# Kernel tuning notes

Hardware: AMD Instinct MI355X
Metric: run time of the kernel (lower is better)

The kernel has to match this reference:

```python
import math
import jax, jax.numpy as jnp
import numpy as np

# Dims (match init_kwargs)
B, S, HID = 2, 2048, 2048
H, KVH, D = 16, 8, 128
ATTN_H = 8                      # softmax heads (head_split_dict)
TN_H = H - ATTN_H               # linear (tnorm) heads
N_REP = H // KVH                # GQA repeat factor
FIRST_TOKENS, LAST_TOKENS = 64, 512  # global prefix + band width for custom mask
EPS = 1e-6
ROPE_BASE = 1e6
SCALE = 1.0 / math.sqrt(D)


def _rope_tables(seq_len):
    inv_freq = 1.0 / (ROPE_BASE ** (jnp.arange(0, D, 2, dtype=jnp.float32) / D))
    t = jnp.arange(seq_len, dtype=jnp.float32)
    freqs = jnp.outer(t, inv_freq)                 # [S, D/2]
    emb = jnp.concatenate([freqs, freqs], axis=-1)  # [S, D]
    return jnp.cos(emb), jnp.sin(emb)


def _rotate_half(x):
    x1, x2 = jnp.split(x, 2, axis=-1)
    return jnp.concatenate([-x2, x1], axis=-1)


def _apply_rope(x, cos, sin):
    # x: [B, h, S, D], cos/sin: [S, D]
    return x * cos[None, None] + _rotate_half(x) * sin[None, None]


def _rms_norm(x):
    # SimpleRMSNorm: computed in fp32, no learned weight
    xf = x.astype(jnp.float32)
    out = xf * jax.lax.rsqrt(jnp.mean(xf * xf, axis=-1, keepdims=True) + EPS)
    return out.astype(x.dtype)


def setup_inputs() -> dict:
    key = jax.random.key(0)
    ks = jax.random.split(key, 6)
    sc = 0.02
    perm_np = np.array([3, 7, 0, 12, 9, 15, 1, 5, 2, 4, 6, 8, 10, 11, 13, 14], np.int32)
    inv_np = np.zeros(H, np.int32)
    inv_np[perm_np] = np.arange(H, dtype=np.int32)
    return {
        'hidden_states': jax.random.normal(ks[0], (B, S, HID), jnp.float32),
        'q_w': jax.random.normal(ks[1], (HID, HID), jnp.float32) * sc,
        'q_b': jnp.zeros((HID,), jnp.float32),
        'k_w': jax.random.normal(ks[2], (KVH * D, HID), jnp.float32) * sc,
        'k_b': jnp.zeros((KVH * D,), jnp.float32),
        'v_w': jax.random.normal(ks[3], (KVH * D, HID), jnp.float32) * sc,
        'v_b': jnp.zeros((KVH * D,), jnp.float32),
        'o_w': jax.random.normal(ks[4], (HID, HID), jnp.float32) * sc,
        'head_policy': jnp.array([1, 0, 1, 0, 1, 0, 1, 0], dtype=bool),
        'perm': jnp.asarray(perm_np),
        'inv_perm': jnp.asarray(inv_np),
    }


def _custom_mask(head_policy):
    # create_custom_causal_mask: banded causal + global prefix for heads with
    # policy==False; plain causal for heads with policy==True. Additive mask.
    qi = jnp.arange(S)[:, None]
    ki = jnp.arange(S)[None, :]
    causal = ki <= qi
    band = causal & ((qi - ki) < LAST_TOKENS)
    band = band | ((ki < FIRST_TOKENS) & (qi >= FIRST_TOKENS))
    neg = jnp.finfo(jnp.float32).min
    orig = jnp.where(causal, 0.0, neg)
    new = jnp.where(band, 0.0, neg)
    return jnp.where(head_policy[:, None, None], orig, new), causal  # [ATTN_H,S,S]


def reference(hidden_states, q_w, q_b, k_w, k_b, v_w, v_b, o_w,
              head_policy, perm, inv_perm):
    dt = hidden_states.dtype
    q = hidden_states @ q_w.T + q_b           # [B,S,HID]
    k = hidden_states @ k_w.T + k_b           # [B,S,KVH*D]
    v = hidden_states @ v_w.T + v_b

    # head permutation on q, then split softmax vs tnorm heads
    q = q.reshape(B, S, H, D)[:, :, perm, :]
    q = jnp.transpose(q, (0, 2, 1, 3))        # [B,H,S,D]
    kh = jnp.transpose(k.reshape(B, S, KVH, D), (0, 2, 1, 3))  # [B,KVH,S,D]
    vh = jnp.transpose(v.reshape(B, S, KVH, D), (0, 2, 1, 3))

    cos, sin = _rope_tables(S)
    q = _apply_rope(q, cos, sin)              # rope on all q heads (both branches)
    kh = _apply_rope(kh, cos, sin)

    # repeat_kv (GQA) then head permutation
    k_all = jnp.repeat(kh, N_REP, axis=1)[:, perm]  # [B,H,S,D]
    v_all = jnp.repeat(vh, N_REP, axis=1)[:, perm]

    # ---- softmax branch (first ATTN_H heads), custom banded/global mask ----
    mask, causal = _custom_mask(head_policy)
    logits = jnp.einsum('bhqd,bhkd->bhqk', q[:, :ATTN_H], k_all[:, :ATTN_H]) * SCALE
    logits = logits + mask[None]
    probs = jax.nn.softmax(logits.astype(jnp.float32), axis=-1).astype(dt)
    out_sm = jnp.einsum('bhqk,bhkd->bhqd', probs, v_all[:, :ATTN_H])
    out_sm = jnp.transpose(out_sm, (0, 2, 1, 3)).reshape(B, S, ATTN_H * D)

    # ---- linear (tnorm) branch (remaining heads): masked qk^T @ v + RMSNorm ----
    w = jnp.einsum('bhqd,bhkd->bhqk', q[:, ATTN_H:], k_all[:, ATTN_H:]) * SCALE
    w = jnp.where(causal[None, None], w, jnp.zeros((), dt))
    out_tn = jnp.einsum('bhqk,bhkd->bhqd', w, v_all[:, ATTN_H:])
    out_tn = jnp.transpose(out_tn, (0, 2, 1, 3)).reshape(B, S, TN_H * D)
    out_tn = _rms_norm(out_tn)

    # concat heads, undo permutation, output projection
    out = jnp.concatenate([out_sm, out_tn], axis=-1)
    out = out.reshape(B, S, H, D)[:, :, inv_perm, :].reshape(B, S, HID)
    return out @ o_w.T
```

## Files before the change

### kernel.cpp

```cpp
#include <hip/hip_runtime.h>
#include <hip/hip_bf16.h>
#include <stdint.h>

#define AS1 __attribute__((address_space(1)))
#define AS3 __attribute__((address_space(3)))

typedef __bf16 bf16x8 __attribute__((ext_vector_type(8)));
typedef unsigned short u16x8 __attribute__((ext_vector_type(8)));
typedef float f32x4 __attribute__((ext_vector_type(4)));

static __device__ __forceinline__ unsigned short f2bf(float f) {
  unsigned u = __float_as_uint(f);
  u += 0x7fffu + ((u >> 16) & 1u);
  return (unsigned short)(u >> 16);
}
static __device__ __forceinline__ float bf2f(unsigned short h) {
  return __uint_as_float(((unsigned)h) << 16);
}
static __device__ __forceinline__ bf16x8 ld_frag(const unsigned short* p) {
  union { u16x8 u; bf16x8 b; } c;
  c.u = *(const u16x8*)p;
  return c.b;
}
static __device__ __forceinline__ void gload16(const void* g, void* l) {
  __builtin_amdgcn_global_load_lds((AS1 const void*)g, (AS3 void*)l, 16, 0, 0);
}
#define MFMA(a, b, c) __builtin_amdgcn_mfma_f32_16x16x32_bf16(a, b, c, 0, 0, 0)
#define BAR asm volatile("s_barrier" ::: "memory")
#define VM4 asm volatile("s_waitcnt vmcnt(4)" ::: "memory")

__global__ __launch_bounds__(256)
void cvt4(const float* __restrict__ in, unsigned short* __restrict__ out, long n) {
  long i = ((long)blockIdx.x * 256 + threadIdx.x) * 4;
  if (i >= n) return;
  float4 f = *(const float4*)&in[i];
  ushort4 u;
  u.x = f2bf(f.x); u.y = f2bf(f.y); u.z = f2bf(f.z); u.w = f2bf(f.w);
  *(ushort4*)&out[i] = u;
}

__global__ __launch_bounds__(256)
void rope_apply(unsigned short* __restrict__ qh, unsigned short* __restrict__ kh) {
  long i = (long)blockIdx.x * 256 + threadIdx.x;
  const long QT = (long)2 * 16 * 2048 * 64;
  unsigned short* p; long rem; float outsc;
  if (i < QT) { p = qh; rem = i; outsc = 0.08838834764831845f; }
  else        { p = kh; rem = i - QT; outsc = 1.0f; }
  int j = (int)(rem & 63);
  long row = rem >> 6;
  int s = (int)(row & 2047);
  unsigned short* x = p + row * 128;
  float inv = exp2f(-0.31143075889569023f * (float)j);
  float f = (float)s * inv;
  float sn, c;
  sincosf(f, &sn, &c);
  float x1 = bf2f(x[j]), x2 = bf2f(x[j + 64]);
  x[j]      = f2bf((x1 * c - x2 * sn) * outsc);
  x[j + 64] = f2bf((x2 * c + x1 * sn) * outsc);
}

__global__ __launch_bounds__(512, 2)
void gemm256_qkv(const unsigned short* __restrict__ A,
                 const unsigned short* __restrict__ Bw,
                 const float* __restrict__ qb, const float* __restrict__ kb,
                 const float* __restrict__ vb,
                 unsigned short* __restrict__ qh, unsigned short* __restrict__ kh,
                 unsigned short* __restrict__ vT) {
  constexpr int K = 2048, NT = K / 64, NIT = NT / 2;
  __shared__ alignas(16) unsigned short LDS[65536];
  const int id = blockIdx.x;
  const int lg = (id & 7) * 32 + (id >> 3);
  const int bm = lg >> 4, bn = lg & 15;
  const int tid = threadIdx.x;
  const int wid = tid >> 6, lane = tid & 63;
  const int wr = wid >> 2, wc = wid & 3;
  const int l15 = lane & 15, lhi = lane >> 4;
  const int rsw = (l15 & 7) << 3;
  const int srow0 = wid * 8 + (lane >> 3);
  const int scol = ((lane & 7) ^ (lane >> 3)) * 8;
  const unsigned short* Ag = A + (long)(bm * 256) * K;
  const unsigned short* Bg = Bw + (long)(bn * 256) * K;
  unsigned short* Al = LDS;
  unsigned short* Bl = LDS + 32768;

#define STG(gb, lb, p, h, t) do {                                              \
    int tc = (t) < NT ? (t) : NT - 1;                                          \
    gload16((gb) + (long)((h) * 128 + srow0) * K + tc * 64 + scol,             \
            (lb) + (p) * 16384 + (h) * 8192 + wid * 512);                      \
    gload16((gb) + (long)((h) * 128 + 64 + srow0) * K + tc * 64 + scol,        \
            (lb) + (p) * 16384 + (h) * 8192 + 4096 + wid * 512);               \
  } while (0)

#define LDA(p, mh) do {                                                        \
    _Pragma("unroll") for (int m4 = 0; m4 < 4; ++m4)                           \
    _Pragma("unroll") for (int kk = 0; kk < 2; ++kk)                           \
      afr[m4][kk] = ld_frag(&Al[(p) * 16384 +                                  \
          (wr * 128 + (mh) * 64 + m4 * 16 + l15) * 64 +                        \
          ((kk * 32 + lhi * 8) ^ rsw)]);                                       \
  } while (0)

#define LDB(p, nh) do {                                                        \
    _Pragma("unroll") for (int n2 = 0; n2 < 2; ++n2)                           \
    _Pragma("unroll") for (int kk = 0; kk < 2; ++kk)                           \
      bfr[nh][n2][kk] = ld_frag(&Bl[(p) * 16384 +                              \
          (wc * 64 + (nh) * 32 + n2 * 16 + l15) * 64 +                         \
          ((kk * 32 + lhi * 8) ^ rsw)]);                                       \
  } while (0)

#define QUAD(mh, nh) do {                                                      \
    __builtin_amdgcn_s_setprio(1);                                             \
    _Pragma("unroll") for (int m4 = 0; m4 < 4; ++m4)                           \
    _Pragma("unroll") for (int n2 = 0; n2 < 2; ++n2)                           \
    _Pragma("unroll") for (int kk = 0; kk < 2; ++kk)                           \
      acc[(mh) * 4 + m4][(nh) * 2 + n2] =                                      \
          MFMA(afr[m4][kk], bfr[nh][n2][kk], acc[(mh) * 4 + m4][(nh) * 2 + n2]);\
    __builtin_amdgcn_s_setprio(0);                                             \
  } while (0)

  f32x4 acc[8][4] = {};
  bf16x8 afr[4][2], bfr[2][2][2];

  STG(Bg, Bl, 0, 0, 0); STG(Bg, Bl, 0, 1, 0);
  STG(Ag, Al, 0, 0, 0); STG(Ag, Al, 0, 1, 0);
  STG(Bg, Bl, 1, 0, 1); STG(Bg, Bl, 1, 1, 1);
  VM4; BAR;

  for (int it = 0; it < NIT; ++it) {
    const int T = 2 * it;
    LDA(0, 0); LDB(0, 0); STG(Ag, Al, 1, 0, T + 1);
    BAR; QUAD(0, 0); BAR;
    LDB(0, 1);            STG(Ag, Al, 1, 1, T + 1);
    BAR; QUAD(0, 1); BAR;
    LDA(0, 1);            STG(Bg, Bl, 0, 0, T + 2);
    BAR; QUAD(1, 0); BAR;
                          STG(Bg, Bl, 0, 1, T + 2);
    VM4; BAR; QUAD(1, 1); BAR;
    LDA(1, 0); LDB(1, 0); STG(Ag, Al, 0, 0, T + 2);
    BAR; QUAD(0, 0); BAR;
    LDB(1, 1);            STG(Ag, Al, 0, 1, T + 2);
    BAR; QUAD(0, 1); BAR;
    LDA(1, 1);            STG(Bg, Bl, 1, 0, T + 3);
    BAR; QUAD(1, 0); BAR;
                          STG(Bg, Bl, 1, 1, T + 3);
    VM4; BAR; QUAD(1, 1); BAR;
  }

  const int r0 = bm * 256 + wr * 128, c0 = bn * 256 + wc * 64;
#pragma unroll
  for (int m = 0; m < 8; ++m) {
#pragma unroll
    for (int n = 0; n < 4; ++n) {
#pragma unroll
      for (int j = 0; j < 4; ++j) {
        int row = r0 + m * 16 + lhi * 4 + j;
        int col = c0 + n * 16 + l15;
        float v = acc[m][n][j];
        int b = row >> 11, s = row & 2047;
        if (col < 2048) {
          v += qb[col];
          qh[((long)(b * 16 + (col >> 7)) * 2048 + s) * 128 + (col & 127)] = f2bf(v);
        } else if (col < 3072) {
          int c = col - 2048; v += kb[c];
          kh[((long)(b * 8 + (c >> 7)) * 2048 + s) * 128 + (c & 127)] = f2bf(v);
        } else {
          int c = col - 3072; v += vb[c];
          vT[((long)(b * 8 + (c >> 7)) * 128 + (c & 127)) * 2048 + s] = f2bf(v);
        }
      }
    }
  }
#undef STG
#undef LDA
#undef LDB
#undef QUAD
}

__global__ __launch_bounds__(256, 2)
void gemm_bt(const unsigned short* __restrict__ A,
             const unsigned short* __restrict__ Bw,
             int K, int N, float* __restrict__ Cout) {
  __shared__ alignas(16) unsigned short As[128 * 64];
  __shared__ alignas(16) unsigned short Bs[128 * 64];
  const int bm = blockIdx.x, bn = blockIdx.y;
  const int tid = threadIdx.x;
  const int w = tid >> 6, l = tid & 63;
  const int wm = w >> 1, wn = w & 1;
  const int l15 = l & 15, lhi = l >> 4;
  f32x4 acc[4][4] = {};
  const unsigned short* aptr = A + ((long)(bm * 128 + w * 8 + (l >> 3))) * K + (l & 7) * 8;
  const unsigned short* bptr = Bw + ((long)(bn * 128 + w * 8 + (l >> 3))) * K + (l & 7) * 8;
  unsigned short* asb = &As[w * 8 * 64];
  unsigned short* bsb = &Bs[w * 8 * 64];
  for (int k0 = 0; k0 < K; k0 += 64) {
#pragma unroll
    for (int i = 0; i < 4; ++i) {
      gload16(aptr + (long)i * 32 * K, asb + i * 2048);
      gload16(bptr + (long)i * 32 * K, bsb + i * 2048);
    }
    aptr += 64; bptr += 64;
    __syncthreads();
#pragma unroll
    for (int kk = 0; kk < 2; ++kk) {
      bf16x8 af[4], bfr[4];
#pragma unroll
      for (int m = 0; m < 4; ++m)
        af[m] = ld_frag(&As[(wm * 64 + m * 16 + l15) * 64 + kk * 32 + lhi * 8]);
#pragma unroll
      for (int n = 0; n < 4; ++n)
        bfr[n] = ld_frag(&Bs[(wn * 64 + n * 16 + l15) * 64 + kk * 32 + lhi * 8]);
#pragma unroll
      for (int m = 0; m < 4; ++m)
#pragma unroll
        for (int n = 0; n < 4; ++n)
          acc[m][n] = MFMA(af[m], bfr[n], acc[m][n]);
    }
    __syncthreads();
  }
#pragma unroll
  for (int m = 0; m < 4; ++m)
#pragma unroll
    for (int n = 0; n < 4; ++n)
#pragma unroll
      for (int j = 0; j < 4; ++j) {
        int row = bm * 128 + wm * 64 + m * 16 + lhi * 4 + j;
        int col = bn * 128 + wn * 64 + n * 16 + l15;
        Cout[(long)row * N + col] = acc[m][n][j];
      }
}

__global__ __launch_bounds__(256, 4)
void attn_all(const unsigned short* __restrict__ qheads,
              const unsigned short* __restrict__ kheads,
              const unsigned short* __restrict__ vT,
              unsigned short* __restrict__ aout,
              unsigned short* __restrict__ tnb,
              const int* __restrict__ perm) {
  __shared__ alignas(16) unsigned short Ks[64 * 128];
  __shared__ alignas(16) unsigned short Vs[128 * 64];
  __shared__ alignas(16) unsigned short Ps[4][16 * 64];
  const int q0 = blockIdx.x * 64;
  const int hy = blockIdx.y;
  const int b = blockIdx.z;
  const bool sm = hy < 8;
  const bool banded = sm && ((hy & 1) != 0);
  const int qhd = perm[hy];
  const int kvh = qhd >> 1;
  const int tid = threadIdx.x, w = tid >> 6, l = tid & 63, l15 = l & 15, lhi = l >> 4;
  const unsigned short* Qg = qheads + ((long)(b * 16 + qhd) * 2048 + q0) * 128;
  const unsigned short* Kg = kheads + (long)(b * 8 + kvh) * 2048 * 128;
  const unsigned short* Vg = vT + (long)(b * 8 + kvh) * 128 * 2048;
  bf16x8 qf[4];
#pragma unroll
  for (int c = 0; c < 4; ++c)
    qf[c] = ld_frag(Qg + (w * 16 + l15) * 128 + c * 32 + lhi * 8);
  f32x4 ao[8] = {};
  float lsum[4] = {0.f, 0.f, 0.f, 0.f};
  const int krow = w * 4 + (l >> 4);
  const long kgoff = (long)krow * 128 + (((l & 15) * 8) ^ ((krow & 7) << 3));
  unsigned short* kdst = &Ks[w * 512];
  const int vrow = w * 8 + (l >> 3);
  const long vgoff = (long)vrow * 2048 + (((l & 7) * 8) ^ ((vrow & 7) << 3));
  unsigned short* vdst = &Vs[w * 512];
  const int rsw15 = (l15 & 7) << 3;

  for (int k0 = 0; k0 <= q0; k0 += 64) {
    if (banded && k0 >= 64 && q0 - k0 >= 575) continue;
    __syncthreads();
#pragma unroll
    for (int p = 0; p < 4; ++p)
      gload16(Kg + (long)(k0 + p * 16) * 128 + kgoff, kdst + p * 2048);
#pragma unroll
    for (int p = 0; p < 4; ++p)
      gload16(Vg + (long)p * 32 * 2048 + k0 + vgoff, vdst + p * 2048);
    __syncthreads();
    f32x4 sacc[4] = {};
#pragma unroll
    for (int c = 0; c < 4; ++c) {
#pragma unroll
      for (int ks = 0; ks < 4; ++ks) {
        bf16x8 kf = ld_frag(&Ks[(ks * 16 + l15) * 128 + ((c * 32 + lhi * 8) ^ rsw15)]);
        sacc[ks] = MFMA(qf[c], kf, sacc[ks]);
      }
    }
    const int qrb = q0 + w * 16 + lhi * 4;
#pragma unroll
    for (int j = 0; j < 4; ++j) {
      const int q = qrb + j;
      const int prow = lhi * 4 + j;
      const int psw = (prow & 7) << 3;
#pragma unroll
      for (int ks = 0; ks < 4; ++ks) {
        int k = k0 + ks * 16 + l15;
        bool ok = (k <= q) && (!banded || k < 64 || (q - k) < 512);
        float p;
        if (sm) { p = ok ? __expf(sacc[ks][j]) : 0.f; lsum[j] += p; }
        else    { p = ok ? sacc[ks][j] : 0.f; }
        Ps[w][prow * 64 + ((ks * 16 + l15) ^ psw)] = f2bf(p);
      }
    }
    bf16x8 pa0 = ld_frag(&Ps[w][l15 * 64 + ((lhi * 8) ^ rsw15)]);
    bf16x8 pa1 = ld_frag(&Ps[w][l15 * 64 + ((32 + lhi * 8) ^ rsw15)]);
#pragma unroll
    for (int n = 0; n < 8; ++n) {
      bf16x8 vf0 = ld_frag(&Vs[(n * 16 + l15) * 64 + ((lhi * 8) ^ rsw15)]);
      bf16x8 vf1 = ld_frag(&Vs[(n * 16 + l15) * 64 + ((32 + lhi * 8) ^ rsw15)]);
      ao[n] = MFMA(pa0, vf0, ao[n]);
      ao[n] = MFMA(pa1, vf1, ao[n]);
    }
  }
  if (sm) {
#pragma unroll
    for (int j = 0; j < 4; ++j) {
      float s = lsum[j];
#pragma unroll
      for (int d = 1; d < 16; d <<= 1) s += __shfl_xor(s, d);
      float inv = 1.0f / s;
      int q = q0 + w * 16 + lhi * 4 + j;
      unsigned short* o = aout + ((long)b * 2048 + q) * 2048 + qhd * 128;
#pragma unroll
      for (int n = 0; n < 8; ++n) o[n * 16 + l15] = f2bf(ao[n][j] * inv);
    }
  } else {
    const int hidx = hy - 8;
#pragma unroll
    for (int j = 0; j < 4; ++j) {
      int q = q0 + w * 16 + lhi * 4 + j;
      unsigned short* o = tnb + ((long)b * 2048 + q) * 1024 + hidx * 128;
#pragma unroll
      for (int n = 0; n < 8; ++n) o[n * 16 + l15] = f2bf(ao[n][j]);
    }
  }
}

__global__ __launch_bounds__(256)
void rms_scatter(const unsigned short* __restrict__ tnb,
                 unsigned short* __restrict__ aout,
                 const int* __restrict__ perm) {
  __shared__ float wsum[4];
  int row = blockIdx.x, tid = threadIdx.x;
  const unsigned short* x = tnb + (long)row * 1024;
  ushort4 u = *(const ushort4*)&x[tid * 4];
  float v0 = bf2f(u.x), v1 = bf2f(u.y), v2 = bf2f(u.z), v3 = bf2f(u.w);
  float ss = v0 * v0 + v1 * v1 + v2 * v2 + v3 * v3;
#pragma unroll
  for (int d = 1; d < 64; d <<= 1) ss += __shfl_xor(ss, d);
  if ((tid & 63) == 0) wsum[tid >> 6] = ss;
  __syncthreads();
  float tot = wsum[0] + wsum[1] + wsum[2] + wsum[3];
  float r = rsqrtf(tot * (1.0f / 1024.0f) + 1e-6f);
  int slot = perm[8 + (tid >> 5)];
  unsigned short* o = aout + (long)row * 2048 + slot * 128 + ((tid * 4) & 127);
  o[0] = f2bf(v0 * r); o[1] = f2bf(v1 * r); o[2] = f2bf(v2 * r); o[3] = f2bf(v3 * r);
}

extern "C" void kernel_launch(void* const* d_in, const int* in_sizes, int n_in,
                              void* d_out, int out_size, void* d_ws, size_t ws_size,
                              hipStream_t stream) {
  const float* hs  = (const float*)d_in[0];
  const float* q_w = (const float*)d_in[1];
  const float* q_b = (const float*)d_in[2];
  const float* k_w = (const float*)d_in[3];
  const float* k_b = (const float*)d_in[4];
  const float* v_w = (const float*)d_in[5];
  const float* v_b = (const float*)d_in[6];
  const float* o_w = (const float*)d_in[7];
  const int* perm  = (const int*)d_in[9];

  char* ws = (char*)d_ws;
  unsigned short* hbf  = (unsigned short*)(ws + 0);
  unsigned short* wqkv = (unsigned short*)(ws + 16777216);
  unsigned short* kh   = (unsigned short*)(ws + 33554432);
  unsigned short* vT   = (unsigned short*)(ws + 41943040);
  unsigned short* qh   = (unsigned short*)d_out;
  unsigned short* aout = hbf;
  unsigned short* tnb  = wqkv;
  unsigned short* owb  = kh;
  float* outF = (float*)d_out;

  cvt4<<<8192, 256, 0, stream>>>(hs, hbf, 8388608);
  cvt4<<<4096, 256, 0, stream>>>(q_w, wqkv, 4194304);
  cvt4<<<2048, 256, 0, stream>>>(k_w, wqkv + 4194304, 2097152);
  cvt4<<<2048, 256, 0, stream>>>(v_w, wqkv + 6291456, 2097152);
  gemm256_qkv<<<256, 512, 0, stream>>>(hbf, wqkv, q_b, k_b, v_b, qh, kh, vT);
  rope_apply<<<24576, 256, 0, stream>>>(qh, kh);
  attn_all<<<dim3(32, 16, 2), 256, 0, stream>>>(qh, kh, vT, aout, tnb, perm);
  cvt4<<<4096, 256, 0, stream>>>(o_w, owb, 4194304);
  rms_scatter<<<4096, 256, 0, stream>>>(tnb, aout, perm);
  gemm_bt<<<dim3(32, 16), 256, 0, stream>>>(aout, owb, 2048, 2048, outF);
}
```

Measured before the change: 285.6 us.

## Double-buffer K/V tiles in attention with async prefetch and reversed block order

The attention kernel now keeps two LDS buffers for K and V. It issues the global-to-LDS load of the next tile before computing on the current one, using vmcnt waits and barriers, so memory latency overlaps with MFMA work. The next tile index jumps directly past the skipped banded region, and query blocks are launched in reverse order so the longest causal rows start first. The larger LDS footprint lowers the launch-bounds occupancy hint from 4 to 2 blocks per CU, which reduces latency hiding through occupancy.

```diff
diff --git a/kernel.cpp b/kernel.cpp
--- a/kernel.cpp
+++ b/kernel.cpp
@@ -27,7 +27,9 @@
 }
 #define MFMA(a, b, c) __builtin_amdgcn_mfma_f32_16x16x32_bf16(a, b, c, 0, 0, 0)
 #define BAR asm volatile("s_barrier" ::: "memory")
+#define VM0 asm volatile("s_waitcnt vmcnt(0)" ::: "memory")
 #define VM4 asm volatile("s_waitcnt vmcnt(4)" ::: "memory")
+#define VM8 asm volatile("s_waitcnt vmcnt(8)" ::: "memory")
 
 __global__ __launch_bounds__(256)
 void cvt4(const float* __restrict__ in, unsigned short* __restrict__ out, long n) {
@@ -228,17 +230,17 @@
       }
 }
 
-__global__ __launch_bounds__(256, 4)
+__global__ __launch_bounds__(256, 2)
 void attn_all(const unsigned short* __restrict__ qheads,
               const unsigned short* __restrict__ kheads,
               const unsigned short* __restrict__ vT,
               unsigned short* __restrict__ aout,
               unsigned short* __restrict__ tnb,
               const int* __restrict__ perm) {
-  __shared__ alignas(16) unsigned short Ks[64 * 128];
-  __shared__ alignas(16) unsigned short Vs[128 * 64];
+  __shared__ alignas(16) unsigned short Ks[2 * 64 * 128];
+  __shared__ alignas(16) unsigned short Vs[2 * 128 * 64];
   __shared__ alignas(16) unsigned short Ps[4][16 * 64];
-  const int q0 = blockIdx.x * 64;
+  const int q0 = (31 - blockIdx.x) * 64;
   const int hy = blockIdx.y;
   const int b = blockIdx.z;
   const bool sm = hy < 8;
@@ -257,28 +259,36 @@
   float lsum[4] = {0.f, 0.f, 0.f, 0.f};
   const int krow = w * 4 + (l >> 4);
   const long kgoff = (long)krow * 128 + (((l & 15) * 8) ^ ((krow & 7) << 3));
-  unsigned short* kdst = &Ks[w * 512];
   const int vrow = w * 8 + (l >> 3);
   const long vgoff = (long)vrow * 2048 + (((l & 7) * 8) ^ ((vrow & 7) << 3));
-  unsigned short* vdst = &Vs[w * 512];
   const int rsw15 = (l15 & 7) << 3;
 
-  for (int k0 = 0; k0 <= q0; k0 += 64) {
-    if (banded && k0 >= 64 && q0 - k0 >= 575) continue;
-    __syncthreads();
-#pragma unroll
-    for (int p = 0; p < 4; ++p)
-      gload16(Kg + (long)(k0 + p * 16) * 128 + kgoff, kdst + p * 2048);
-#pragma unroll
-    for (int p = 0; p < 4; ++p)
-      gload16(Vg + (long)p * 32 * 2048 + k0 + vgoff, vdst + p * 2048);
-    __syncthreads();
+#define STAGE(bf, k0) do {                                                     \
+    unsigned short* kd = &Ks[(bf) * 8192 + w * 512];                           \
+    unsigned short* vd = &Vs[(bf) * 8192 + w * 512];                           \
+    _Pragma("unroll") for (int p = 0; p < 4; ++p)                              \
+      gload16(Kg + (long)((k0) + p * 16) * 128 + kgoff, kd + p * 2048);        \
+    _Pragma("unroll") for (int p = 0; p < 4; ++p)                              \
+      gload16(Vg + (long)p * 32 * 2048 + (k0) + vgoff, vd + p * 2048);         \
+  } while (0)
+
+#define NXT(k0) (banded && ((k0) + 64) >= 64 && (q0 - ((k0) + 64)) >= 575      \
+                     ? (q0 - 512) : ((k0) + 64))
+
+  STAGE(0, 0);
+  VM0; BAR;
+  int cur = 0;
+  for (int k0 = 0; k0 <= q0; ) {
+    const int k1 = NXT(k0);
+    if (k1 <= q0) { STAGE(cur ^ 1, k1); VM8; } else { VM0; }
+    BAR;
+    const int kb = cur * 8192;
     f32x4 sacc[4] = {};
 #pragma unroll
     for (int c = 0; c < 4; ++c) {
 #pragma unroll
       for (int ks = 0; ks < 4; ++ks) {
-        bf16x8 kf = ld_frag(&Ks[(ks * 16 + l15) * 128 + ((c * 32 + lhi * 8) ^ rsw15)]);
+        bf16x8 kf = ld_frag(&Ks[kb + (ks * 16 + l15) * 128 + ((c * 32 + lhi * 8) ^ rsw15)]);
         sacc[ks] = MFMA(qf[c], kf, sacc[ks]);
       }
     }
@@ -302,12 +312,16 @@
     bf16x8 pa1 = ld_frag(&Ps[w][l15 * 64 + ((32 + lhi * 8) ^ rsw15)]);
 #pragma unroll
     for (int n = 0; n < 8; ++n) {
-      bf16x8 vf0 = ld_frag(&Vs[(n * 16 + l15) * 64 + ((lhi * 8) ^ rsw15)]);
-      bf16x8 vf1 = ld_frag(&Vs[(n * 16 + l15) * 64 + ((32 + lhi * 8) ^ rsw15)]);
+      bf16x8 vf0 = ld_frag(&Vs[kb + (n * 16 + l15) * 64 + ((lhi * 8) ^ rsw15)]);
+      bf16x8 vf1 = ld_frag(&Vs[kb + (n * 16 + l15) * 64 + ((32 + lhi * 8) ^ rsw15)]);
       ao[n] = MFMA(pa0, vf0, ao[n]);
       ao[n] = MFMA(pa1, vf1, ao[n]);
     }
+    BAR;
+    k0 = k1; cur ^= 1;
   }
+#undef STAGE
+#undef NXT
   if (sm) {
 #pragma unroll
     for (int j = 0; j < 4; ++j) {
```

Result: slower. 341.3 us (+19.5%).

## Replace output-projection GEMM with 256x256 double-buffered pipelined kernel

Applied to the files above, without the earlier changes.

Replaces the simple 128x128 output-projection GEMM with a 512-thread, 256x256-tile kernel. It double-buffers K-tiles in LDS with XOR swizzling, interleaves global-to-LDS staging with quarter-tile MFMA phases, and remaps block IDs for locality. MFMA sections in both the GEMM and the attention kernel are wrapped in s_setprio raises to favour matrix issue. The aim is to hide global-load latency and raise data reuse, at the cost of only 128 blocks in the grid, which may underfill the device.

```diff
diff --git a/kernel.cpp b/kernel.cpp
--- a/kernel.cpp
+++ b/kernel.cpp
@@ -175,57 +175,104 @@
 #undef QUAD
 }
 
-__global__ __launch_bounds__(256, 2)
-void gemm_bt(const unsigned short* __restrict__ A,
-             const unsigned short* __restrict__ Bw,
-             int K, int N, float* __restrict__ Cout) {
-  __shared__ alignas(16) unsigned short As[128 * 64];
-  __shared__ alignas(16) unsigned short Bs[128 * 64];
-  const int bm = blockIdx.x, bn = blockIdx.y;
+__global__ __launch_bounds__(512, 2)
+void gemm256_o(const unsigned short* __restrict__ A,
+               const unsigned short* __restrict__ Bw,
+               float* __restrict__ Cout) {
+  constexpr int K = 2048, NT = K / 64, NIT = NT / 2;
+  __shared__ alignas(16) unsigned short LDS[65536];
+  const int id = blockIdx.x;
+  const int lg = (id & 7) * 16 + (id >> 3);
+  const int bm = lg >> 3, bn = lg & 7;
   const int tid = threadIdx.x;
-  const int w = tid >> 6, l = tid & 63;
-  const int wm = w >> 1, wn = w & 1;
-  const int l15 = l & 15, lhi = l >> 4;
-  f32x4 acc[4][4] = {};
-  const unsigned short* aptr = A + ((long)(bm * 128 + w * 8 + (l >> 3))) * K + (l & 7) * 8;
-  const unsigned short* bptr = Bw + ((long)(bn * 128 + w * 8 + (l >> 3))) * K + (l & 7) * 8;
-  unsigned short* asb = &As[w * 8 * 64];
-  unsigned short* bsb = &Bs[w * 8 * 64];
-  for (int k0 = 0; k0 < K; k0 += 64) {
-#pragma unroll
-    for (int i = 0; i < 4; ++i) {
-      gload16(aptr + (long)i * 32 * K, asb + i * 2048);
-      gload16(bptr + (long)i * 32 * K, bsb + i * 2048);
-    }
-    aptr += 64; bptr += 64;
-    __syncthreads();
-#pragma unroll
-    for (int kk = 0; kk < 2; ++kk) {
-      bf16x8 af[4], bfr[4];
-#pragma unroll
-      for (int m = 0; m < 4; ++m)
-        af[m] = ld_frag(&As[(wm * 64 + m * 16 + l15) * 64 + kk * 32 + lhi * 8]);
-#pragma unroll
-      for (int n = 0; n < 4; ++n)
-        bfr[n] = ld_frag(&Bs[(wn * 64 + n * 16 + l15) * 64 + kk * 32 + lhi * 8]);
-#pragma unroll
-      for (int m = 0; m < 4; ++m)
-#pragma unroll
-        for (int n = 0; n < 4; ++n)
-          acc[m][n] = MFMA(af[m], bfr[n], acc[m][n]);
-    }
-    __syncthreads();
+  const int wid = tid >> 6, lane = tid & 63;
+  const int wr = wid >> 2, wc = wid & 3;
+  const int l15 = lane & 15, lhi = lane >> 4;
+  const int rsw = (l15 & 7) << 3;
+  const int srow0 = wid * 8 + (lane >> 3);
+  const int scol = ((lane & 7) ^ (lane >> 3)) * 8;
+  const unsigned short* Ag = A + (long)(bm * 256) * K;
+  const unsigned short* Bg = Bw + (long)(bn * 256) * K;
+  unsigned short* Al = LDS;
+  unsigned short* Bl = LDS + 32768;
+
+#define STG(gb, lb, p, h, t) do {                                              \
+    int tc = (t) < NT ? (t) : NT - 1;                                          \
+    gload16((gb) + (long)((h) * 128 + srow0) * K + tc * 64 + scol,             \
+            (lb) + (p) * 16384 + (h) * 8192 + wid * 512);                      \
+    gload16((gb) + (long)((h) * 128 + 64 + srow0) * K + tc * 64 + scol,        \
+            (lb) + (p) * 16384 + (h) * 8192 + 4096 + wid * 512);               \
+  } while (0)
+
+#define LDA(p, mh) do {                                                        \
+    _Pragma("unroll") for (int m4 = 0; m4 < 4; ++m4)                           \
+    _Pragma("unroll") for (int kk = 0; kk < 2; ++kk)                           \
+      afr[m4][kk] = ld_frag(&Al[(p) * 16384 +                                  \
+          (wr * 128 + (mh) * 64 + m4 * 16 + l15) * 64 +                        \
+          ((kk * 32 + lhi * 8) ^ rsw)]);                                       \
+  } while (0)
+
+#define LDB(p, nh) do {                                                        \
+    _Pragma("unroll") for (int n2 = 0; n2 < 2; ++n2)                           \
+    _Pragma("unroll") for (int kk = 0; kk < 2; ++kk)                           \
+      bfr[nh][n2][kk] = ld_frag(&Bl[(p) * 16384 +                              \
+          (wc * 64 + (nh) * 32 + n2 * 16 + l15) * 64 +                         \
+          ((kk * 32 + lhi * 8) ^ rsw)]);                                       \
+  } while (0)
+
+#define QUAD(mh, nh) do {                                                      \
+    __builtin_amdgcn_s_setprio(1);                                             \
+    _Pragma("unroll") for (int m4 = 0; m4 < 4; ++m4)                           \
+    _Pragma("unroll") for (int n2 = 0; n2 < 2; ++n2)                           \
+    _Pragma("unroll") for (int kk = 0; kk < 2; ++kk)                           \
+      acc[(mh) * 4 + m4][(nh) * 2 + n2] =                                      \
+          MFMA(afr[m4][kk], bfr[nh][n2][kk], acc[(mh) * 4 + m4][(nh) * 2 + n2]);\
+    __builtin_amdgcn_s_setprio(0);                                             \
+  } while (0)
+
+  f32x4 acc[8][4] = {};
+  bf16x8 afr[4][2], bfr[2][2][2];
+
+  STG(Bg, Bl, 0, 0, 0); STG(Bg, Bl, 0, 1, 0);
+  STG(Ag, Al, 0, 0, 0); STG(Ag, Al, 0, 1, 0);
+  STG(Bg, Bl, 1, 0, 1); STG(Bg, Bl, 1, 1, 1);
+  VM4; BAR;
+
+  for (int it = 0; it < NIT; ++it) {
+    const int T = 2 * it;
+    LDA(0, 0); LDB(0, 0); STG(Ag, Al, 1, 0, T + 1);
+    BAR; QUAD(0, 0); BAR;
+    LDB(0, 1);            STG(Ag, Al, 1, 1, T + 1);
+    BAR; QUAD(0, 1); BAR;
+    LDA(0, 1);            STG(Bg, Bl, 0, 0, T + 2);
+    BAR; QUAD(1, 0); BAR;
+                          STG(Bg, Bl, 0, 1, T + 2);
+    VM4; BAR; QUAD(1, 1); BAR;
+    LDA(1, 0); LDB(1, 0); STG(Ag, Al, 0, 0, T + 2);
+    BAR; QUAD(0, 0); BAR;
+    LDB(1, 1);            STG(Ag, Al, 0, 1, T + 2);
+    BAR; QUAD(0, 1); BAR;
+    LDA(1, 1);            STG(Bg, Bl, 1, 0, T + 3);
+    BAR; QUAD(1, 0); BAR;
+                          STG(Bg, Bl, 1, 1, T + 3);
+    VM4; BAR; QUAD(1, 1); BAR;
   }
-#pragma unroll
-  for (int m = 0; m < 4; ++m)
+
+  const int r0 = bm * 256 + wr * 128, c0 = bn * 256 + wc * 64;
+#pragma unroll
+  for (int m = 0; m < 8; ++m)
 #pragma unroll
     for (int n = 0; n < 4; ++n)
 #pragma unroll
       for (int j = 0; j < 4; ++j) {
-        int row = bm * 128 + wm * 64 + m * 16 + lhi * 4 + j;
-        int col = bn * 128 + wn * 64 + n * 16 + l15;
-        Cout[(long)row * N + col] = acc[m][n][j];
+        int row = r0 + m * 16 + lhi * 4 + j;
+        int col = c0 + n * 16 + l15;
+        Cout[(long)row * 2048 + col] = acc[m][n][j];
       }
+#undef STG
+#undef LDA
+#undef LDB
+#undef QUAD
 }
 
 __global__ __launch_bounds__(256, 4)
@@ -274,6 +321,7 @@
       gload16(Vg + (long)p * 32 * 2048 + k0 + vgoff, vdst + p * 2048);
     __syncthreads();
     f32x4 sacc[4] = {};
+    __builtin_amdgcn_s_setprio(1);
 #pragma unroll
     for (int c = 0; c < 4; ++c) {
 #pragma unroll
@@ -282,6 +330,7 @@
         sacc[ks] = MFMA(qf[c], kf, sacc[ks]);
       }
     }
+    __builtin_amdgcn_s_setprio(0);
     const int qrb = q0 + w * 16 + lhi * 4;
 #pragma unroll
     for (int j = 0; j < 4; ++j) {
@@ -300,6 +349,7 @@
     }
     bf16x8 pa0 = ld_frag(&Ps[w][l15 * 64 + ((lhi * 8) ^ rsw15)]);
     bf16x8 pa1 = ld_frag(&Ps[w][l15 * 64 + ((32 + lhi * 8) ^ rsw15)]);
+    __builtin_amdgcn_s_setprio(1);
 #pragma unroll
     for (int n = 0; n < 8; ++n) {
       bf16x8 vf0 = ld_frag(&Vs[(n * 16 + l15) * 64 + ((lhi * 8) ^ rsw15)]);
@@ -307,6 +357,7 @@
       ao[n] = MFMA(pa0, vf0, ao[n]);
       ao[n] = MFMA(pa1, vf1, ao[n]);
     }
+    __builtin_amdgcn_s_setprio(0);
   }
   if (sm) {
 #pragma unroll
@@ -386,5 +437,5 @@
   attn_all<<<dim3(32, 16, 2), 256, 0, stream>>>(qh, kh, vT, aout, tnb, perm);
   cvt4<<<4096, 256, 0, stream>>>(o_w, owb, 4194304);
   rms_scatter<<<4096, 256, 0, stream>>>(tnb, aout, perm);
-  gemm_bt<<<dim3(32, 16), 256, 0, stream>>>(aout, owb, 2048, 2048, outF);
-}
+  gemm256_o<<<128, 512, 0, stream>>>(aout, owb, outF);
+}
```

New measurement: 288.6 us. Within noise of the previous version (+1.1%).
